# Kernel tuning notes

Measured on AMD Instinct MI355X. Metric: run time of the kernel, lower is better.

Reference implementation:

```python
import jax, jax.numpy as jnp
import numpy as np
import math

E = 256          # embed_dims
H = 8            # num_heads
ITER = 2         # iterative steps
PC_RANGE = (-140.8, -40.0, -3.0, 140.8, 40.0, 1.0)


def sine_embed(pos, num_feats):
    # pos: (..., 3) in (0,1); returns (..., 3*num_feats), per-coord interleaved sin/cos
    scale = 2.0 * math.pi
    i = jnp.arange(num_feats, dtype=jnp.float32)
    dim_t = 10000.0 ** (2.0 * jnp.floor(i / 2.0) / num_feats)
    p = pos[..., None] * scale / dim_t                      # (..., 3, F)
    emb = jnp.stack([jnp.sin(p[..., 0::2]), jnp.cos(p[..., 1::2])], axis=-1)
    emb = emb.reshape(p.shape[:-1] + (num_feats,))          # (..., 3, F)
    return emb.reshape(pos.shape[:-1] + (3 * num_feats,))


def mha(q, k, v, Wi, bi, Wo, bo, n_heads):
    # torch nn.MultiheadAttention math, seq-first layout: q (L,N,C), k/v (M,N,C)
    L, N, C = q.shape
    D = C // n_heads
    qp = (q @ Wi[:C].T + bi[:C]).reshape(L, N, n_heads, D)
    kp = (k @ Wi[C:2 * C].T + bi[C:2 * C]).reshape(k.shape[0], N, n_heads, D)
    vp = (v @ Wi[2 * C:].T + bi[2 * C:]).reshape(v.shape[0], N, n_heads, D)
    scores = jnp.einsum('lnhd,mnhd->nhlm', qp, kp) / math.sqrt(D)
    attn = jax.nn.softmax(scores, axis=-1)
    o = jnp.einsum('nhlm,mnhd->lnhd', attn, vp).reshape(L, N, C)
    return o @ Wo.T + bo


def setup_inputs() -> dict:
    key = jax.random.key(0)
    ks = jax.random.split(key, 12)
    Q, TOT, B, LMAX = 2048, 40, 8, 5
    s = 0.02
    return {
        'x': jax.random.normal(ks[0], (Q, TOT, E), jnp.float32),
        'reference_points': jax.random.uniform(ks[1], (TOT, Q, 3), jnp.float32),
        'pairwise_t_matrix': jax.random.normal(ks[2], (B, LMAX, LMAX, 4, 4), jnp.float32),
        'record_len': np.full((B,), 5, dtype=np.int64),
        'in_proj_w': jax.random.normal(ks[3], (3 * E, E), jnp.float32) * s,
        'in_proj_b': jnp.zeros((3 * E,), jnp.float32),
        'out_w': jax.random.normal(ks[4], (E, E), jnp.float32) * s,
        'out_b': jnp.zeros((E,), jnp.float32),
        'bev_w1': jax.random.normal(ks[5], (E, 3 * E), jnp.float32) * s,
        'bev_b1': jnp.zeros((E,), jnp.float32),
        'bev_w2': jax.random.normal(ks[6], (E, E), jnp.float32) * s,
        'bev_b2': jnp.zeros((E,), jnp.float32),
    }


def reference(x, reference_points, pairwise_t_matrix, in_proj_w, in_proj_b,
              out_w, out_b, bev_w1, bev_b1, bev_w2, bev_b2, record_len):
    rl = np.asarray(record_len)
    offsets = np.concatenate([[0], np.cumsum(rl)]).astype(int)
    lo = jnp.asarray(PC_RANGE[:3], jnp.float32)
    hi = jnp.asarray(PC_RANGE[3:], jnp.float32)

    x_cav = jnp.transpose(x, (1, 0, 2))                    # (total_cav, Q, C)
    ref = reference_points * (hi - lo) + lo                # un-normalize to pc_range

    outs = []
    for b in range(len(rl)):
        s, e = offsets[b], offsets[b + 1]
        n = e - s
        b_x = x_cav[s:e]                                   # (n, Q, C)
        if n == 1:
            outs.append(b_x)
            continue
        b_ref = ref[s:e]                                   # (n, Q, 3)
        t_ego = pairwise_t_matrix[b, :n, 0]                # (n, 4, 4) transform-to-ego
        homo = jnp.concatenate([b_ref, jnp.ones(b_ref.shape[:-1] + (1,), b_ref.dtype)], axis=-1)
        trans = jax.nn.sigmoid(jnp.einsum('nij,nqj->nqi', t_ego, homo)[..., :3])
        pe = sine_embed(trans, E)                          # (n, Q, 3E)
        bev = jax.nn.relu(pe @ bev_w1.T + bev_b1) @ bev_w2.T + bev_b2  # (n, Q, C)

        ego = b_x[0:1]
        neigh = b_x[1:]                                    # (n-1, Q, C)
        kk = neigh + bev[1:]
        for _ in range(ITER):
            q = jnp.broadcast_to(ego, neigh.shape)
            o = q + mha(q, kk, neigh, in_proj_w, in_proj_b, out_w, out_b, H)
            ego = jnp.sum(o, axis=0, keepdims=True)
        outs.append(jnp.concatenate([ego, neigh], axis=0))

    out = jnp.concatenate(outs, axis=0)                    # (total_cav, Q, C)
    return jnp.transpose(out, (1, 0, 2))                   # (Q, total_cav, C)
```

## Files before the change

### kernel.cpp

```cpp
#include <hip/hip_runtime.h>
#include <cstdint>
#include <cstddef>

typedef __bf16 bf16;
typedef __attribute__((ext_vector_type(8))) __bf16 bf16x8;
typedef __attribute__((ext_vector_type(4))) float f32x4;
typedef __attribute__((ext_vector_type(4))) unsigned int u32x4;

#define QN 2048

#if __has_builtin(__builtin_amdgcn_sinf)
#define SIN_REV(x) __builtin_amdgcn_sinf(x)
#define COS_REV(x) __builtin_amdgcn_cosf(x)
#else
#define SIN_REV(x) __sinf((x) * 6.283185307179586f)
#define COS_REV(x) __cosf((x) * 6.283185307179586f)
#endif

__device__ __forceinline__ float sigmoidf_(float v) { return 1.0f / (1.0f + __expf(-v)); }

__device__ __forceinline__ bf16x8 cvt8(const float* p) {
  const f32x4* p4 = (const f32x4*)p;
  f32x4 lo = p4[0], hi = p4[1];
  bf16x8 r;
#pragma unroll
  for (int j = 0; j < 4; ++j) { r[j] = (bf16)lo[j]; r[j + 4] = (bf16)hi[j]; }
  return r;
}

__device__ __forceinline__ void load_lds16(const bf16* g, bf16* l) {
  __builtin_amdgcn_global_load_lds(
      (const __attribute__((address_space(1))) void*)g,
      (__attribute__((address_space(3))) void*)l, 16, 0, 0);
}

__global__ __launch_bounds__(256) void copy_ker(const u32x4* __restrict__ in,
                                                u32x4* __restrict__ out, int n) {
  int i = blockIdx.x * 256 + threadIdx.x;
  if (i >= n) return;
  int t = (i >> 6) % 40;
  if ((t % 5) == 0) return;
  out[i] = in[i];
}

__global__ __launch_bounds__(256) void cvtw_ker(const float* __restrict__ ipw,
                                                const float* __restrict__ ow,
                                                const float* __restrict__ w1,
                                                const float* __restrict__ w2,
                                                bf16* __restrict__ wb) {
  int e = (blockIdx.x * 256 + threadIdx.x) * 8;
  const float* src; int off;
  if (e < 196608)      { src = ipw; off = e; }
  else if (e < 262144) { src = ow;  off = e - 196608; }
  else if (e < 458752) { src = w1;  off = e - 262144; }
  else                 { src = w2;  off = e - 458752; }
  *(bf16x8*)(wb + e) = cvt8(src + off);
}

__global__ __launch_bounds__(256) void wcomb_ker(const float* __restrict__ ipw,
                                                 const float* __restrict__ ipb,
                                                 const float* __restrict__ w2f,
                                                 const float* __restrict__ b2f,
                                                 bf16* __restrict__ Wc,
                                                 float* __restrict__ bkf) {
  __shared__ float row[256];
  __shared__ float red[256];
  const int j = blockIdx.x, l = threadIdx.x;
  row[l] = ipw[65536 + j * 256 + l];
  __syncthreads();
  float acc = 0.f;
#pragma unroll 4
  for (int m = 0; m < 256; ++m) acc += row[m] * w2f[m * 256 + l];
  Wc[(size_t)j * 512 + l] = (bf16)acc;
  Wc[(size_t)j * 512 + 256 + l] = (bf16)row[l];
  red[l] = row[l] * b2f[l];
  __syncthreads();
  for (int s = 128; s > 0; s >>= 1) {
    if (l < s) red[l] += red[l + s];
    __syncthreads();
  }
  if (l == 0) bkf[j] = ipb[256 + j] + red[0];
}

template <int AMODE, int EPI, int KDIM>
__global__ __launch_bounds__(256) void gemm_ker(
    const bf16* __restrict__ A, const float* __restrict__ Af,
    const bf16* __restrict__ W, const float* __restrict__ bias,
    const float* __restrict__ x, const float* __restrict__ rp,
    const float* __restrict__ pm, const float* __restrict__ egoPrev,
    bf16* __restrict__ outB, float* __restrict__ outF) {
  __shared__ bf16 As[128][40];
  __shared__ bf16 Bs[128][32];

  const int tid = threadIdx.x;
  const int bidm = blockIdx.x >> 1;
  const int bidn = blockIdx.x & 1;
  const int rowBase = bidm << 7;
  const int colBase = bidn << 7;

  const int wave = tid >> 6, lane = tid & 63;
  const int m16 = lane & 15, quad = lane >> 4;
  const int wr = wave >> 1, wc = wave & 1;

  const int sRow = tid >> 1, sHalf = tid & 1;
  const int rgA = rowBase + sRow;

  const float* afp = nullptr;
  float tr0 = 0.f, tr1 = 0.f, tr2 = 0.f;
  if constexpr (AMODE == 1) {
    int b = rgA >> 13, j = (rgA >> 11) & 3, q = rgA & 2047;
    int t = b * 5 + 1 + j;
    const float* rpp = rp + ((size_t)t * QN + q) * 3;
    float r0 = rpp[0] * 281.6f - 140.8f;
    float r1 = rpp[1] * 80.0f - 40.0f;
    float r2 = rpp[2] * 4.0f - 3.0f;
    const float* T = pm + (size_t)t * 80;
    tr0 = sigmoidf_(T[0] * r0 + T[1] * r1 + T[2] * r2 + T[3]);
    tr1 = sigmoidf_(T[4] * r0 + T[5] * r1 + T[6] * r2 + T[7]);
    tr2 = sigmoidf_(T[8] * r0 + T[9] * r1 + T[10] * r2 + T[11]);
  } else if constexpr (AMODE == 2 || AMODE == 5) {
    int b = rgA >> 13, j = (rgA >> 11) & 3, q = rgA & 2047;
    afp = x + (((size_t)q * 40 + b * 5 + 1 + j) << 8);
  } else if constexpr (AMODE == 3) {
    int b = rgA >> 11, q = rgA & 2047;
    afp = x + (((size_t)q * 40 + b * 5) << 8);
  } else if constexpr (AMODE == 4) {
    afp = Af + (size_t)rgA * 256;
  }

  const bf16* wsrc = W + (size_t)(colBase + (wave << 5) + (lane >> 2)) * KDIM + ((lane & 3) << 3);
  bf16* bdst0 = &Bs[(wave << 5)][0];
  bf16* bdst1 = &Bs[(wave << 5) + 16][0];

  f32x4 acc[4][4] = {};

  for (int k0 = 0; k0 < KDIM; k0 += 32) {
    load_lds16(wsrc + k0, bdst0);
    load_lds16(wsrc + (size_t)16 * KDIM + k0, bdst1);

    bf16x8 a0, a1;
    if constexpr (AMODE == 1) {
      int c = k0 >> 8;
      float tc = (c == 0) ? tr0 : (c == 1 ? tr1 : tr2);
      int ti0 = ((k0 & 255) + (sHalf << 4)) >> 1;
      float freq = exp2f((float)ti0 * -0.10381025296522975f);
#pragma unroll
      for (int p = 0; p < 4; ++p) {
        float ang = tc * freq;
        a0[2 * p]     = (bf16)SIN_REV(ang);
        a0[2 * p + 1] = (bf16)COS_REV(ang);
        freq *= 0.93057204092467f;
      }
#pragma unroll
      for (int p = 0; p < 4; ++p) {
        float ang = tc * freq;
        a1[2 * p]     = (bf16)SIN_REV(ang);
        a1[2 * p + 1] = (bf16)COS_REV(ang);
        freq *= 0.93057204092467f;
      }
    } else if constexpr (AMODE == 0) {
      const bf16* ap = A + (size_t)rgA * KDIM + k0 + (sHalf << 4);
      a0 = ((const bf16x8*)ap)[0];
      a1 = ((const bf16x8*)ap)[1];
    } else if constexpr (AMODE == 5) {
      if (k0 < 256) {
        const bf16* ap = A + ((size_t)rgA << 8) + k0 + (sHalf << 4);
        a0 = ((const bf16x8*)ap)[0];
        a1 = ((const bf16x8*)ap)[1];
      } else {
        const float* fp = afp + (k0 - 256) + (sHalf << 4);
        a0 = cvt8(fp);
        a1 = cvt8(fp + 8);
      }
    } else {
      const float* fp = afp + k0 + (sHalf << 4);
      a0 = cvt8(fp);
      a1 = cvt8(fp + 8);
    }
    *(bf16x8*)(&As[sRow][sHalf << 4]) = a0;
    *(bf16x8*)(&As[sRow][(sHalf << 4) + 8]) = a1;
    __syncthreads();

    bf16x8 afr[4], bfr[4];
#pragma unroll
    for (int mt = 0; mt < 4; ++mt)
      afr[mt] = *(const bf16x8*)(&As[(wr << 6) + (mt << 4) + m16][quad << 3]);
#pragma unroll
    for (int nt = 0; nt < 4; ++nt)
      bfr[nt] = *(const bf16x8*)(&Bs[(wc << 6) + (nt << 4) + m16][quad << 3]);
#pragma unroll
    for (int mt = 0; mt < 4; ++mt)
#pragma unroll
      for (int nt = 0; nt < 4; ++nt)
        acc[mt][nt] = __builtin_amdgcn_mfma_f32_16x16x32_bf16(
            afr[mt], bfr[nt], acc[mt][nt], 0, 0, 0);
    __syncthreads();
  }

#pragma unroll
  for (int mt = 0; mt < 4; ++mt) {
#pragma unroll
    for (int nt = 0; nt < 4; ++nt) {
      const int col = colBase + (wc << 6) + (nt << 4) + m16;
      const float bv = bias[col];
#pragma unroll
      for (int rg = 0; rg < 4; ++rg) {
        const int r = rowBase + (wr << 6) + (mt << 4) + (quad << 2) + rg;
        float v = acc[mt][nt][rg] + bv;
        if constexpr (EPI == 0) {
          outB[(size_t)r * 256 + col] = (bf16)fmaxf(v, 0.0f);
        } else if constexpr (EPI == 1) {
          int b = r >> 13, j = (r >> 11) & 3, q = r & 2047;
          v += x[(((size_t)q * 40 + b * 5 + 1 + j) << 8) + col];
          outB[(size_t)r * 256 + col] = (bf16)v;
        } else if constexpr (EPI == 2) {
          outB[(size_t)r * 256 + col] = (bf16)v;
        } else if constexpr (EPI == 3) {
          int b = r >> 11, q = r & 2047;
          float xe = x[(((size_t)q * 40 + b * 5) << 8) + col];
          outF[(size_t)r * 256 + col] = 4.0f * (xe + v);
        } else if constexpr (EPI == 4) {
          int b = r >> 11, q = r & 2047;
          float e1 = egoPrev[(size_t)r * 256 + col];
          outF[(((size_t)q * 40 + b * 5) << 8) + col] = 4.0f * (e1 + v);
        }
      }
    }
  }
}

__global__ __launch_bounds__(256) void attn_ker(const bf16* __restrict__ qp,
                                                const bf16* __restrict__ kp,
                                                const bf16* __restrict__ vp,
                                                bf16* __restrict__ o) {
  int p = blockIdx.x * 256 + threadIdx.x;
  int h = p & 7;
  int re = p >> 3;
  int b = re >> 11;
  int q = re & 2047;
  const bf16x8* qpv = (const bf16x8*)(qp + ((size_t)re << 8) + h * 32);
  float qv[32];
#pragma unroll
  for (int i = 0; i < 4; ++i) {
    bf16x8 t = qpv[i];
#pragma unroll
    for (int j = 0; j < 8; ++j) qv[i * 8 + j] = (float)t[j];
  }
  size_t base = ((size_t)(b * 4) * QN + q) * 256 + h * 32;
  float s[4];
#pragma unroll
  for (int m = 0; m < 4; ++m) {
    const bf16x8* kv = (const bf16x8*)(kp + base + (size_t)m * (QN * 256));
    float a = 0.f;
#pragma unroll
    for (int i = 0; i < 4; ++i) {
      bf16x8 t = kv[i];
#pragma unroll
      for (int j = 0; j < 8; ++j) a += qv[i * 8 + j] * (float)t[j];
    }
    s[m] = a * 0.17677669529663687f;
  }
  float mx = fmaxf(fmaxf(s[0], s[1]), fmaxf(s[2], s[3]));
  float e0 = __expf(s[0] - mx), e1 = __expf(s[1] - mx);
  float e2 = __expf(s[2] - mx), e3 = __expf(s[3] - mx);
  float inv = 1.0f / (e0 + e1 + e2 + e3);
  float w[4] = {e0 * inv, e1 * inv, e2 * inv, e3 * inv};
  float ov[32] = {};
#pragma unroll
  for (int m = 0; m < 4; ++m) {
    const bf16x8* vv = (const bf16x8*)(vp + base + (size_t)m * (QN * 256));
#pragma unroll
    for (int i = 0; i < 4; ++i) {
      bf16x8 t = vv[i];
#pragma unroll
      for (int j = 0; j < 8; ++j) ov[i * 8 + j] += w[m] * (float)t[j];
    }
  }
  bf16x8* op = (bf16x8*)(o + ((size_t)re << 8) + h * 32);
#pragma unroll
  for (int i = 0; i < 4; ++i) {
    bf16x8 t;
#pragma unroll
    for (int j = 0; j < 8; ++j) t[j] = (bf16)ov[i * 8 + j];
    op[i] = t;
  }
}

extern "C" void kernel_launch(void* const* d_in, const int* in_sizes, int n_in,
                              void* d_out, int out_size, void* d_ws, size_t ws_size,
                              hipStream_t stream) {
  (void)n_in; (void)out_size; (void)ws_size;
  const float* x   = (const float*)d_in[0];
  const float* rp  = (const float*)d_in[1];
  const float* pm  = (const float*)d_in[2];
  const int wbase = (in_sizes[3] == 8) ? 4 : 3;
  const float* ipw = (const float*)d_in[wbase + 0];
  const float* ipb = (const float*)d_in[wbase + 1];
  const float* ow  = (const float*)d_in[wbase + 2];
  const float* obv = (const float*)d_in[wbase + 3];
  const float* w1  = (const float*)d_in[wbase + 4];
  const float* b1  = (const float*)d_in[wbase + 5];
  const float* w2  = (const float*)d_in[wbase + 6];
  const float* b2  = (const float*)d_in[wbase + 7];
  float* out = (float*)d_out;
  char* ws = (char*)d_ws;

  bf16* h    = (bf16*)(ws + 0);
  bf16* qp   = (bf16*)(ws + 0);
  bf16* oo   = (bf16*)(ws + 8388608);
  bf16* kp   = (bf16*)(ws + 33554432);
  bf16* vp   = (bf16*)(ws + 67108864);
  float* egoF = (float*)(ws + 100663296);
  bf16* wb   = (bf16*)(ws + 117440512);
  bf16* Wc   = (bf16*)(ws + 118489088);
  float* bkf = (float*)(ws + 118751232);
  const bf16* wq  = wb;
  const bf16* wv  = wb + 131072;
  const bf16* owb = wb + 196608;
  const bf16* w1b = wb + 262144;

  cvtw_ker<<<256, 256, 0, stream>>>(ipw, ow, w1, w2, wb);
  wcomb_ker<<<256, 256, 0, stream>>>(ipw, ipb, w2, b2, Wc, bkf);
  copy_ker<<<20480, 256, 0, stream>>>((const u32x4*)x, (u32x4*)out, 5242880);
  gemm_ker<1, 0, 768><<<1024, 256, 0, stream>>>(nullptr, nullptr, w1b, b1, x, rp, pm, nullptr, h, nullptr);
  gemm_ker<5, 2, 512><<<1024, 256, 0, stream>>>(h, nullptr, Wc, bkf, x, rp, pm, nullptr, kp, nullptr);
  gemm_ker<2, 2, 256><<<1024, 256, 0, stream>>>(nullptr, nullptr, wv, ipb + 512, x, rp, pm, nullptr, vp, nullptr);
  gemm_ker<3, 2, 256><<<256, 256, 0, stream>>>(nullptr, nullptr, wq, ipb, x, rp, pm, nullptr, qp, nullptr);
  attn_ker<<<512, 256, 0, stream>>>(qp, kp, vp, oo);
  gemm_ker<0, 3, 256><<<256, 256, 0, stream>>>(oo, nullptr, owb, obv, x, rp, pm, nullptr, nullptr, egoF);
  gemm_ker<4, 2, 256><<<256, 256, 0, stream>>>(nullptr, egoF, wq, ipb, x, rp, pm, nullptr, qp, nullptr);
  attn_ker<<<512, 256, 0, stream>>>(qp, kp, vp, oo);
  gemm_ker<0, 4, 256><<<256, 256, 0, stream>>>(oo, nullptr, owb, obv, x, rp, pm, egoF, nullptr, out);
}
```

Baseline: 382.7 us.

## Build sine-embedding A fragments in registers for the PE GEMM, bypassing LDS

Replaces the generic GEMM's AMODE 1 path with a dedicated kernel for the positional-embedding MLP. Each lane generates its sin/cos values directly in MFMA A-fragment layout and reads weight fragments straight from global memory, so the kernel needs no LDS staging and no barriers. It also stops converting the unused w2 weight to bf16. The cost is duplicated transcendental work: both column-half waves compute the same rows. Weight reads now depend on cache behaviour rather than coalesced LDS staging.

```diff
diff --git a/kernel.cpp b/kernel.cpp
--- a/kernel.cpp
+++ b/kernel.cpp
@@ -46,14 +46,12 @@
 __global__ __launch_bounds__(256) void cvtw_ker(const float* __restrict__ ipw,
                                                 const float* __restrict__ ow,
                                                 const float* __restrict__ w1,
-                                                const float* __restrict__ w2,
                                                 bf16* __restrict__ wb) {
   int e = (blockIdx.x * 256 + threadIdx.x) * 8;
   const float* src; int off;
   if (e < 196608)      { src = ipw; off = e; }
   else if (e < 262144) { src = ow;  off = e - 196608; }
-  else if (e < 458752) { src = w1;  off = e - 262144; }
-  else                 { src = w2;  off = e - 458752; }
+  else                 { src = w1;  off = e - 262144; }
   *(bf16x8*)(wb + e) = cvt8(src + off);
 }
 
@@ -82,6 +80,91 @@
   if (l == 0) bkf[j] = ipb[256 + j] + red[0];
 }
 
+__global__ __launch_bounds__(256) void pe_gemm_ker(
+    const bf16* __restrict__ W, const float* __restrict__ bias,
+    const float* __restrict__ rp, const float* __restrict__ pm,
+    bf16* __restrict__ outB) {
+  const int tid = threadIdx.x;
+  const int bidm = blockIdx.x >> 1;
+  const int bidn = blockIdx.x & 1;
+  const int rowBase = bidm << 7;
+  const int colBase = bidn << 7;
+  const int wave = tid >> 6, lane = tid & 63;
+  const int m16 = lane & 15, quad = lane >> 4;
+  const int wr = wave >> 1, wc = wave & 1;
+
+  float tr[3][4];
+#pragma unroll
+  for (int mt = 0; mt < 4; ++mt) {
+    int r = rowBase + (wr << 6) + (mt << 4) + m16;
+    int b = r >> 13, j = (r >> 11) & 3, q = r & 2047;
+    int t = b * 5 + 1 + j;
+    const float* rpp = rp + ((size_t)t * QN + q) * 3;
+    float r0 = rpp[0] * 281.6f - 140.8f;
+    float r1 = rpp[1] * 80.0f - 40.0f;
+    float r2 = rpp[2] * 4.0f - 3.0f;
+    const float* T = pm + (size_t)t * 80;
+    tr[0][mt] = sigmoidf_(T[0] * r0 + T[1] * r1 + T[2] * r2 + T[3]);
+    tr[1][mt] = sigmoidf_(T[4] * r0 + T[5] * r1 + T[6] * r2 + T[7]);
+    tr[2][mt] = sigmoidf_(T[8] * r0 + T[9] * r1 + T[10] * r2 + T[11]);
+  }
+
+  const bf16* bsrc = W + (size_t)(colBase + (wc << 6) + m16) * 768 + (quad << 3);
+
+  const float freq0 = exp2f((float)(quad << 2) * -0.10381025296522975f);
+  const float R = 0.9305720409296979f;
+  const float R16 = 0.31622776601683794f;
+
+  f32x4 acc[4][4] = {};
+
+#pragma unroll
+  for (int c = 0; c < 3; ++c) {
+    float fq = freq0;
+#pragma unroll
+    for (int s = 0; s < 8; ++s) {
+      const int k0 = (c << 8) + (s << 5);
+      bf16x8 bfr[4];
+#pragma unroll
+      for (int nt = 0; nt < 4; ++nt)
+        bfr[nt] = *(const bf16x8*)(bsrc + (size_t)(nt << 4) * 768 + k0);
+      const float f0 = fq, f1 = f0 * R, f2 = f1 * R, f3 = f2 * R;
+      bf16x8 afr[4];
+#pragma unroll
+      for (int mt = 0; mt < 4; ++mt) {
+        const float tc = tr[c][mt];
+        const float a0 = tc * f0, a1 = tc * f1, a2 = tc * f2, a3 = tc * f3;
+        afr[mt][0] = (bf16)SIN_REV(a0); afr[mt][1] = (bf16)COS_REV(a0);
+        afr[mt][2] = (bf16)SIN_REV(a1); afr[mt][3] = (bf16)COS_REV(a1);
+        afr[mt][4] = (bf16)SIN_REV(a2); afr[mt][5] = (bf16)COS_REV(a2);
+        afr[mt][6] = (bf16)SIN_REV(a3); afr[mt][7] = (bf16)COS_REV(a3);
+      }
+#pragma unroll
+      for (int mt = 0; mt < 4; ++mt)
+#pragma unroll
+        for (int nt = 0; nt < 4; ++nt)
+          acc[mt][nt] = __builtin_amdgcn_mfma_f32_16x16x32_bf16(
+              afr[mt], bfr[nt], acc[mt][nt], 0, 0, 0);
+      fq = f3 * R * R16 / R16;
+      fq = f0 * R16;
+    }
+  }
+
+#pragma unroll
+  for (int mt = 0; mt < 4; ++mt) {
+#pragma unroll
+    for (int nt = 0; nt < 4; ++nt) {
+      const int col = colBase + (wc << 6) + (nt << 4) + m16;
+      const float bv = bias[col];
+#pragma unroll
+      for (int rg = 0; rg < 4; ++rg) {
+        const int r = rowBase + (wr << 6) + (mt << 4) + (quad << 2) + rg;
+        float v = acc[mt][nt][rg] + bv;
+        outB[(size_t)r * 256 + col] = (bf16)fmaxf(v, 0.0f);
+      }
+    }
+  }
+}
+
 template <int AMODE, int EPI, int KDIM>
 __global__ __launch_bounds__(256) void gemm_ker(
     const bf16* __restrict__ A, const float* __restrict__ Af,
@@ -106,19 +189,7 @@
   const int rgA = rowBase + sRow;
 
   const float* afp = nullptr;
-  float tr0 = 0.f, tr1 = 0.f, tr2 = 0.f;
-  if constexpr (AMODE == 1) {
-    int b = rgA >> 13, j = (rgA >> 11) & 3, q = rgA & 2047;
-    int t = b * 5 + 1 + j;
-    const float* rpp = rp + ((size_t)t * QN + q) * 3;
-    float r0 = rpp[0] * 281.6f - 140.8f;
-    float r1 = rpp[1] * 80.0f - 40.0f;
-    float r2 = rpp[2] * 4.0f - 3.0f;
-    const float* T = pm + (size_t)t * 80;
-    tr0 = sigmoidf_(T[0] * r0 + T[1] * r1 + T[2] * r2 + T[3]);
-    tr1 = sigmoidf_(T[4] * r0 + T[5] * r1 + T[6] * r2 + T[7]);
-    tr2 = sigmoidf_(T[8] * r0 + T[9] * r1 + T[10] * r2 + T[11]);
-  } else if constexpr (AMODE == 2 || AMODE == 5) {
+  if constexpr (AMODE == 2 || AMODE == 5) {
     int b = rgA >> 13, j = (rgA >> 11) & 3, q = rgA & 2047;
     afp = x + (((size_t)q * 40 + b * 5 + 1 + j) << 8);
   } else if constexpr (AMODE == 3) {
@@ -139,26 +210,7 @@
     load_lds16(wsrc + (size_t)16 * KDIM + k0, bdst1);
 
     bf16x8 a0, a1;
-    if constexpr (AMODE == 1) {
-      int c = k0 >> 8;
-      float tc = (c == 0) ? tr0 : (c == 1 ? tr1 : tr2);
-      int ti0 = ((k0 & 255) + (sHalf << 4)) >> 1;
-      float freq = exp2f((float)ti0 * -0.10381025296522975f);
-#pragma unroll
-      for (int p = 0; p < 4; ++p) {
-        float ang = tc * freq;
-        a0[2 * p]     = (bf16)SIN_REV(ang);
-        a0[2 * p + 1] = (bf16)COS_REV(ang);
-        freq *= 0.93057204092467f;
-      }
-#pragma unroll
-      for (int p = 0; p < 4; ++p) {
-        float ang = tc * freq;
-        a1[2 * p]     = (bf16)SIN_REV(ang);
-        a1[2 * p + 1] = (bf16)COS_REV(ang);
-        freq *= 0.93057204092467f;
-      }
-    } else if constexpr (AMODE == 0) {
+    if constexpr (AMODE == 0) {
       const bf16* ap = A + (size_t)rgA * KDIM + k0 + (sHalf << 4);
       a0 = ((const bf16x8*)ap)[0];
       a1 = ((const bf16x8*)ap)[1];
@@ -209,10 +261,6 @@
         float v = acc[mt][nt][rg] + bv;
         if constexpr (EPI == 0) {
           outB[(size_t)r * 256 + col] = (bf16)fmaxf(v, 0.0f);
-        } else if constexpr (EPI == 1) {
-          int b = r >> 13, j = (r >> 11) & 3, q = r & 2047;
-          v += x[(((size_t)q * 40 + b * 5 + 1 + j) << 8) + col];
-          outB[(size_t)r * 256 + col] = (bf16)v;
         } else if constexpr (EPI == 2) {
           outB[(size_t)r * 256 + col] = (bf16)v;
         } else if constexpr (EPI == 3) {
@@ -319,10 +367,10 @@
   const bf16* owb = wb + 196608;
   const bf16* w1b = wb + 262144;
 
-  cvtw_ker<<<256, 256, 0, stream>>>(ipw, ow, w1, w2, wb);
+  cvtw_ker<<<224, 256, 0, stream>>>(ipw, ow, w1, wb);
   wcomb_ker<<<256, 256, 0, stream>>>(ipw, ipb, w2, b2, Wc, bkf);
   copy_ker<<<20480, 256, 0, stream>>>((const u32x4*)x, (u32x4*)out, 5242880);
-  gemm_ker<1, 0, 768><<<1024, 256, 0, stream>>>(nullptr, nullptr, w1b, b1, x, rp, pm, nullptr, h, nullptr);
+  pe_gemm_ker<<<1024, 256, 0, stream>>>(w1b, b1, rp, pm, h);
   gemm_ker<5, 2, 512><<<1024, 256, 0, stream>>>(h, nullptr, Wc, bkf, x, rp, pm, nullptr, kp, nullptr);
   gemm_ker<2, 2, 256><<<1024, 256, 0, stream>>>(nullptr, nullptr, wv, ipb + 512, x, rp, pm, nullptr, vp, nullptr);
   gemm_ker<3, 2, 256><<<256, 256, 0, stream>>>(nullptr, nullptr, wq, ipb, x, rp, pm, nullptr, qp, nullptr);
```

Measured after the change: 414.7 us. 8.4% more time.

## Double-buffer GEMM with 256x64 tiles, XOR-swizzled LDS, and fuse x copy into V projection

Applied to the files above, without the earlier changes.

The GEMM kernel now uses 256x64 block tiles with a K-step of 64 and double-buffered, XOR-swizzled LDS. The next A/B slice is fetched into registers while MFMAs run on the current buffer, which halves barriers per K and is meant to hide global latency and avoid LDS bank conflicts. The separate copy kernel that wrote the neighbor rows of x into the output is removed. The V-projection GEMM now writes those fp32 rows while it reads them, and the unused w2 conversion is dropped. Costs are higher register pressure (launch_bounds 256,2) and larger LDS use, which may limit occupancy.

```diff
diff --git a/kernel.cpp b/kernel.cpp
--- a/kernel.cpp
+++ b/kernel.cpp
@@ -28,32 +28,28 @@
   return r;
 }
 
+__device__ __forceinline__ bf16x8 cvt8v(f32x4 lo, f32x4 hi) {
+  bf16x8 r;
+#pragma unroll
+  for (int j = 0; j < 4; ++j) { r[j] = (bf16)lo[j]; r[j + 4] = (bf16)hi[j]; }
+  return r;
+}
+
 __device__ __forceinline__ void load_lds16(const bf16* g, bf16* l) {
   __builtin_amdgcn_global_load_lds(
       (const __attribute__((address_space(1))) void*)g,
       (__attribute__((address_space(3))) void*)l, 16, 0, 0);
 }
 
-__global__ __launch_bounds__(256) void copy_ker(const u32x4* __restrict__ in,
-                                                u32x4* __restrict__ out, int n) {
-  int i = blockIdx.x * 256 + threadIdx.x;
-  if (i >= n) return;
-  int t = (i >> 6) % 40;
-  if ((t % 5) == 0) return;
-  out[i] = in[i];
-}
-
 __global__ __launch_bounds__(256) void cvtw_ker(const float* __restrict__ ipw,
                                                 const float* __restrict__ ow,
                                                 const float* __restrict__ w1,
-                                                const float* __restrict__ w2,
                                                 bf16* __restrict__ wb) {
   int e = (blockIdx.x * 256 + threadIdx.x) * 8;
   const float* src; int off;
   if (e < 196608)      { src = ipw; off = e; }
   else if (e < 262144) { src = ow;  off = e - 196608; }
-  else if (e < 458752) { src = w1;  off = e - 262144; }
-  else                 { src = w2;  off = e - 458752; }
+  else                 { src = w1;  off = e - 262144; }
   *(bf16x8*)(wb + e) = cvt8(src + off);
 }
 
@@ -82,28 +78,30 @@
   if (l == 0) bkf[j] = ipb[256 + j] + red[0];
 }
 
-template <int AMODE, int EPI, int KDIM>
-__global__ __launch_bounds__(256) void gemm_ker(
+template <int AMODE, int EPI, int KDIM, bool COPYX>
+__global__ __launch_bounds__(256, 2) void gemm_ker(
     const bf16* __restrict__ A, const float* __restrict__ Af,
     const bf16* __restrict__ W, const float* __restrict__ bias,
     const float* __restrict__ x, const float* __restrict__ rp,
     const float* __restrict__ pm, const float* __restrict__ egoPrev,
     bf16* __restrict__ outB, float* __restrict__ outF) {
-  __shared__ bf16 As[128][40];
-  __shared__ bf16 Bs[128][32];
+  __shared__ bf16 As[2][256][64];
+  __shared__ bf16 Bs[2][64][64];
+
+  constexpr int NS = KDIM / 64;
 
   const int tid = threadIdx.x;
-  const int bidm = blockIdx.x >> 1;
-  const int bidn = blockIdx.x & 1;
-  const int rowBase = bidm << 7;
-  const int colBase = bidn << 7;
+  const int bidm = blockIdx.x >> 2;
+  const int bidn = blockIdx.x & 3;
+  const int rowBase = bidm << 8;
+  const int colBase = bidn << 6;
 
   const int wave = tid >> 6, lane = tid & 63;
   const int m16 = lane & 15, quad = lane >> 4;
-  const int wr = wave >> 1, wc = wave & 1;
-
-  const int sRow = tid >> 1, sHalf = tid & 1;
-  const int rgA = rowBase + sRow;
+  const int sA = m16 & 7;
+  const int sT = tid & 7;
+
+  const int rgA = rowBase + tid;
 
   const float* afp = nullptr;
   float tr0 = 0.f, tr1 = 0.f, tr2 = 0.f;
@@ -127,92 +125,125 @@
   } else if constexpr (AMODE == 4) {
     afp = Af + (size_t)rgA * 256;
   }
-
-  const bf16* wsrc = W + (size_t)(colBase + (wave << 5) + (lane >> 2)) * KDIM + ((lane & 3) << 3);
-  bf16* bdst0 = &Bs[(wave << 5)][0];
-  bf16* bdst1 = &Bs[(wave << 5) + 16][0];
+  float* dstX = nullptr;
+  if constexpr (COPYX) dstX = outF + (afp - x);
+
+#define STAGE_B(PP, KO)                                                       \
+  {                                                                           \
+    _Pragma("unroll") for (int i_ = 0; i_ < 2; ++i_) {                        \
+      int rg_ = (wave << 3) + (i_ << 5) + (lane >> 3);                        \
+      const bf16* src_ = W + (size_t)(colBase + rg_) * KDIM + (KO) +          \
+                         (((lane & 7) ^ (lane >> 3)) << 3);                   \
+      load_lds16(src_, &Bs[(PP)][(wave << 3) + (i_ << 5)][0]);                \
+    }                                                                         \
+  }
+
+#define FETCH_A(KO)                                                           \
+  if constexpr (AMODE == 0) {                                                 \
+    _Pragma("unroll") for (int j_ = 0; j_ < 8; ++j_)                          \
+        aB[j_] = ((const bf16x8*)(A + (size_t)rgA * KDIM + (KO)))[j_];        \
+  } else if constexpr (AMODE == 5) {                                          \
+    if ((KO) < 256) {                                                         \
+      _Pragma("unroll") for (int j_ = 0; j_ < 8; ++j_)                        \
+          aB[j_] = ((const bf16x8*)(A + ((size_t)rgA << 8) + (KO)))[j_];      \
+    } else {                                                                  \
+      _Pragma("unroll") for (int j_ = 0; j_ < 16; ++j_)                       \
+          aF[j_] = ((const f32x4*)(afp + (KO) - 256))[j_];                    \
+    }                                                                         \
+  } else if constexpr (AMODE != 1) {                                          \
+    _Pragma("unroll") for (int j_ = 0; j_ < 16; ++j_)                         \
+        aF[j_] = ((const f32x4*)(afp + (KO)))[j_];                            \
+  }
+
+#define FINISH_A(PP, KO)                                                      \
+  {                                                                           \
+    bf16x8 v_[8];                                                             \
+    if constexpr (AMODE == 1) {                                               \
+      const int c_ = (KO) >> 8;                                               \
+      const float tc_ = (c_ == 0) ? tr0 : (c_ == 1 ? tr1 : tr2);              \
+      float fr_ = exp2f((float)(((KO) & 255) >> 1) * -0.10381025296522975f);  \
+      _Pragma("unroll") for (int js_ = 0; js_ < 32; ++js_) {                  \
+        float a_ = tc_ * fr_;                                                 \
+        v_[js_ >> 2][(js_ & 3) * 2] = (bf16)SIN_REV(a_);                      \
+        v_[js_ >> 2][(js_ & 3) * 2 + 1] = (bf16)COS_REV(a_);                  \
+        fr_ *= 0.9305720409296979f;                                           \
+      }                                                                       \
+    } else if constexpr (AMODE == 0) {                                        \
+      _Pragma("unroll") for (int j_ = 0; j_ < 8; ++j_) v_[j_] = aB[j_];       \
+    } else if constexpr (AMODE == 5) {                                        \
+      if ((KO) < 256) {                                                       \
+        _Pragma("unroll") for (int j_ = 0; j_ < 8; ++j_) v_[j_] = aB[j_];     \
+      } else {                                                                \
+        _Pragma("unroll") for (int j_ = 0; j_ < 8; ++j_)                      \
+            v_[j_] = cvt8v(aF[2 * j_], aF[2 * j_ + 1]);                       \
+      }                                                                       \
+    } else {                                                                  \
+      _Pragma("unroll") for (int j_ = 0; j_ < 8; ++j_)                        \
+          v_[j_] = cvt8v(aF[2 * j_], aF[2 * j_ + 1]);                         \
+      if constexpr (COPYX) {                                                  \
+        _Pragma("unroll") for (int j_ = 0; j_ < 16; ++j_)                     \
+            ((f32x4*)(dstX + (KO)))[j_] = aF[j_];                             \
+      }                                                                       \
+    }                                                                         \
+    _Pragma("unroll") for (int j_ = 0; j_ < 8; ++j_)                          \
+        *(bf16x8*)(&As[(PP)][tid][(j_ ^ sT) << 3]) = v_[j_];                  \
+  }
 
   f32x4 acc[4][4] = {};
 
-  for (int k0 = 0; k0 < KDIM; k0 += 32) {
-    load_lds16(wsrc + k0, bdst0);
-    load_lds16(wsrc + (size_t)16 * KDIM + k0, bdst1);
-
-    bf16x8 a0, a1;
-    if constexpr (AMODE == 1) {
-      int c = k0 >> 8;
-      float tc = (c == 0) ? tr0 : (c == 1 ? tr1 : tr2);
-      int ti0 = ((k0 & 255) + (sHalf << 4)) >> 1;
-      float freq = exp2f((float)ti0 * -0.10381025296522975f);
-#pragma unroll
-      for (int p = 0; p < 4; ++p) {
-        float ang = tc * freq;
-        a0[2 * p]     = (bf16)SIN_REV(ang);
-        a0[2 * p + 1] = (bf16)COS_REV(ang);
-        freq *= 0.93057204092467f;
-      }
-#pragma unroll
-      for (int p = 0; p < 4; ++p) {
-        float ang = tc * freq;
-        a1[2 * p]     = (bf16)SIN_REV(ang);
-        a1[2 * p + 1] = (bf16)COS_REV(ang);
-        freq *= 0.93057204092467f;
-      }
-    } else if constexpr (AMODE == 0) {
-      const bf16* ap = A + (size_t)rgA * KDIM + k0 + (sHalf << 4);
-      a0 = ((const bf16x8*)ap)[0];
-      a1 = ((const bf16x8*)ap)[1];
-    } else if constexpr (AMODE == 5) {
-      if (k0 < 256) {
-        const bf16* ap = A + ((size_t)rgA << 8) + k0 + (sHalf << 4);
-        a0 = ((const bf16x8*)ap)[0];
-        a1 = ((const bf16x8*)ap)[1];
-      } else {
-        const float* fp = afp + (k0 - 256) + (sHalf << 4);
-        a0 = cvt8(fp);
-        a1 = cvt8(fp + 8);
-      }
-    } else {
-      const float* fp = afp + k0 + (sHalf << 4);
-      a0 = cvt8(fp);
-      a1 = cvt8(fp + 8);
-    }
-    *(bf16x8*)(&As[sRow][sHalf << 4]) = a0;
-    *(bf16x8*)(&As[sRow][(sHalf << 4) + 8]) = a1;
+  {
+    f32x4 aF[16]; bf16x8 aB[8];
+    FETCH_A(0);
+    STAGE_B(0, 0);
+    FINISH_A(0, 0);
+  }
+  __syncthreads();
+
+#pragma unroll
+  for (int t = 0; t < NS; ++t) {
+    const int p = t & 1;
+    const int kn = (t + 1) << 6;
+    f32x4 aF[16]; bf16x8 aB[8];
+    if (t + 1 < NS) {
+      FETCH_A(kn);
+      STAGE_B(p ^ 1, kn);
+    }
+#pragma unroll
+    for (int kk = 0; kk < 2; ++kk) {
+      const int ks = (((kk << 2) + quad) ^ sA) << 3;
+      bf16x8 afr[4], bfr[4];
+#pragma unroll
+      for (int mt = 0; mt < 4; ++mt)
+        afr[mt] = *(const bf16x8*)(&As[p][(wave << 6) + (mt << 4) + m16][ks]);
+#pragma unroll
+      for (int nt = 0; nt < 4; ++nt)
+        bfr[nt] = *(const bf16x8*)(&Bs[p][(nt << 4) + m16][ks]);
+#pragma unroll
+      for (int mt = 0; mt < 4; ++mt)
+#pragma unroll
+        for (int nt = 0; nt < 4; ++nt)
+          acc[mt][nt] = __builtin_amdgcn_mfma_f32_16x16x32_bf16(
+              afr[mt], bfr[nt], acc[mt][nt], 0, 0, 0);
+    }
+    if (t + 1 < NS) FINISH_A(p ^ 1, kn);
     __syncthreads();
-
-    bf16x8 afr[4], bfr[4];
-#pragma unroll
-    for (int mt = 0; mt < 4; ++mt)
-      afr[mt] = *(const bf16x8*)(&As[(wr << 6) + (mt << 4) + m16][quad << 3]);
-#pragma unroll
-    for (int nt = 0; nt < 4; ++nt)
-      bfr[nt] = *(const bf16x8*)(&Bs[(wc << 6) + (nt << 4) + m16][quad << 3]);
-#pragma unroll
-    for (int mt = 0; mt < 4; ++mt)
-#pragma unroll
-      for (int nt = 0; nt < 4; ++nt)
-        acc[mt][nt] = __builtin_amdgcn_mfma_f32_16x16x32_bf16(
-            afr[mt], bfr[nt], acc[mt][nt], 0, 0, 0);
-    __syncthreads();
-  }
+  }
+#undef STAGE_B
+#undef FETCH_A
+#undef FINISH_A
 
 #pragma unroll
   for (int mt = 0; mt < 4; ++mt) {
 #pragma unroll
     for (int nt = 0; nt < 4; ++nt) {
-      const int col = colBase + (wc << 6) + (nt << 4) + m16;
+      const int col = colBase + (nt << 4) + m16;
       const float bv = bias[col];
 #pragma unroll
       for (int rg = 0; rg < 4; ++rg) {
-        const int r = rowBase + (wr << 6) + (mt << 4) + (quad << 2) + rg;
+        const int r = rowBase + (wave << 6) + (mt << 4) + (quad << 2) + rg;
         float v = acc[mt][nt][rg] + bv;
         if constexpr (EPI == 0) {
           outB[(size_t)r * 256 + col] = (bf16)fmaxf(v, 0.0f);
-        } else if constexpr (EPI == 1) {
-          int b = r >> 13, j = (r >> 11) & 3, q = r & 2047;
-          v += x[(((size_t)q * 40 + b * 5 + 1 + j) << 8) + col];
-          outB[(size_t)r * 256 + col] = (bf16)v;
         } else if constexpr (EPI == 2) {
           outB[(size_t)r * 256 + col] = (bf16)v;
         } else if constexpr (EPI == 3) {
@@ -319,16 +350,22 @@
   const bf16* owb = wb + 196608;
   const bf16* w1b = wb + 262144;
 
-  cvtw_ker<<<256, 256, 0, stream>>>(ipw, ow, w1, w2, wb);
+  cvtw_ker<<<224, 256, 0, stream>>>(ipw, ow, w1, wb);
   wcomb_ker<<<256, 256, 0, stream>>>(ipw, ipb, w2, b2, Wc, bkf);
-  copy_ker<<<20480, 256, 0, stream>>>((const u32x4*)x, (u32x4*)out, 5242880);
-  gemm_ker<1, 0, 768><<<1024, 256, 0, stream>>>(nullptr, nullptr, w1b, b1, x, rp, pm, nullptr, h, nullptr);
-  gemm_ker<5, 2, 512><<<1024, 256, 0, stream>>>(h, nullptr, Wc, bkf, x, rp, pm, nullptr, kp, nullptr);
-  gemm_ker<2, 2, 256><<<1024, 256, 0, stream>>>(nullptr, nullptr, wv, ipb + 512, x, rp, pm, nullptr, vp, nullptr);
-  gemm_ker<3, 2, 256><<<256, 256, 0, stream>>>(nullptr, nullptr, wq, ipb, x, rp, pm, nullptr, qp, nullptr);
+  gemm_ker<1, 0, 768, false><<<1024, 256, 0, stream>>>(
+      nullptr, nullptr, w1b, b1, x, rp, pm, nullptr, h, nullptr);
+  gemm_ker<5, 2, 512, false><<<1024, 256, 0, stream>>>(
+      h, nullptr, Wc, bkf, x, rp, pm, nullptr, kp, nullptr);
+  gemm_ker<2, 2, 256, true><<<1024, 256, 0, stream>>>(
+      nullptr, nullptr, wv, ipb + 512, x, rp, pm, nullptr, vp, out);
+  gemm_ker<3, 2, 256, false><<<256, 256, 0, stream>>>(
+      nullptr, nullptr, wq, ipb, x, rp, pm, nullptr, qp, nullptr);
   attn_ker<<<512, 256, 0, stream>>>(qp, kp, vp, oo);
-  gemm_ker<0, 3, 256><<<256, 256, 0, stream>>>(oo, nullptr, owb, obv, x, rp, pm, nullptr, nullptr, egoF);
-  gemm_ker<4, 2, 256><<<256, 256, 0, stream>>>(nullptr, egoF, wq, ipb, x, rp, pm, nullptr, qp, nullptr);
+  gemm_ker<0, 3, 256, false><<<256, 256, 0, stream>>>(
+      oo, nullptr, owb, obv, x, rp, pm, nullptr, nullptr, egoF);
+  gemm_ker<4, 2, 256, false><<<256, 256, 0, stream>>>(
+      nullptr, egoF, wq, ipb, x, rp, pm, nullptr, qp, nullptr);
   attn_ker<<<512, 256, 0, stream>>>(qp, kp, vp, oo);
-  gemm_ker<0, 4, 256><<<256, 256, 0, stream>>>(oo, nullptr, owb, obv, x, rp, pm, egoF, nullptr, out);
-}
+  gemm_ker<0, 4, 256, false><<<256, 256, 0, stream>>>(
+      oo, nullptr, owb, obv, x, rp, pm, egoF, nullptr, out);
+}
```

Result: slower. 519.8 us (+35.8%).

## Fuse both attention iterations into one kernel with LDS-resident ego rows

Applied to the files above, without the earlier changes.

Replaces the per-iteration sequence of Q-projection GEMM, attention kernel, output-projection GEMM (six launches) with a single kernel. Each block holds 32 ego rows in swizzled LDS and runs the q projection, attention, out projection and residual for both iterations. This removes the global round trips for qp, attention output and the ego intermediate, along with the launch overheads. In exchange, the small 32-row tiles reduce MFMA reuse of the weights, each block reloads the full weight matrices four times, and LDS usage is higher. The w2 conversion is dropped from the weight-conversion kernel because it was unused.

```diff
diff --git a/kernel.cpp b/kernel.cpp
--- a/kernel.cpp
+++ b/kernel.cpp
@@ -46,14 +46,12 @@
 __global__ __launch_bounds__(256) void cvtw_ker(const float* __restrict__ ipw,
                                                 const float* __restrict__ ow,
                                                 const float* __restrict__ w1,
-                                                const float* __restrict__ w2,
                                                 bf16* __restrict__ wb) {
   int e = (blockIdx.x * 256 + threadIdx.x) * 8;
   const float* src; int off;
   if (e < 196608)      { src = ipw; off = e; }
   else if (e < 262144) { src = ow;  off = e - 196608; }
-  else if (e < 458752) { src = w1;  off = e - 262144; }
-  else                 { src = w2;  off = e - 458752; }
+  else                 { src = w1;  off = e - 262144; }
   *(bf16x8*)(wb + e) = cvt8(src + off);
 }
 
@@ -84,11 +82,10 @@
 
 template <int AMODE, int EPI, int KDIM>
 __global__ __launch_bounds__(256) void gemm_ker(
-    const bf16* __restrict__ A, const float* __restrict__ Af,
-    const bf16* __restrict__ W, const float* __restrict__ bias,
-    const float* __restrict__ x, const float* __restrict__ rp,
-    const float* __restrict__ pm, const float* __restrict__ egoPrev,
-    bf16* __restrict__ outB, float* __restrict__ outF) {
+    const bf16* __restrict__ A, const bf16* __restrict__ W,
+    const float* __restrict__ bias, const float* __restrict__ x,
+    const float* __restrict__ rp, const float* __restrict__ pm,
+    bf16* __restrict__ outB) {
   __shared__ bf16 As[128][40];
   __shared__ bf16 Bs[128][32];
 
@@ -121,11 +118,6 @@
   } else if constexpr (AMODE == 2 || AMODE == 5) {
     int b = rgA >> 13, j = (rgA >> 11) & 3, q = rgA & 2047;
     afp = x + (((size_t)q * 40 + b * 5 + 1 + j) << 8);
-  } else if constexpr (AMODE == 3) {
-    int b = rgA >> 11, q = rgA & 2047;
-    afp = x + (((size_t)q * 40 + b * 5) << 8);
-  } else if constexpr (AMODE == 4) {
-    afp = Af + (size_t)rgA * 256;
   }
 
   const bf16* wsrc = W + (size_t)(colBase + (wave << 5) + (lane >> 2)) * KDIM + ((lane & 3) << 3);
@@ -209,44 +201,60 @@
         float v = acc[mt][nt][rg] + bv;
         if constexpr (EPI == 0) {
           outB[(size_t)r * 256 + col] = (bf16)fmaxf(v, 0.0f);
-        } else if constexpr (EPI == 1) {
-          int b = r >> 13, j = (r >> 11) & 3, q = r & 2047;
-          v += x[(((size_t)q * 40 + b * 5 + 1 + j) << 8) + col];
+        } else {
           outB[(size_t)r * 256 + col] = (bf16)v;
-        } else if constexpr (EPI == 2) {
-          outB[(size_t)r * 256 + col] = (bf16)v;
-        } else if constexpr (EPI == 3) {
-          int b = r >> 11, q = r & 2047;
-          float xe = x[(((size_t)q * 40 + b * 5) << 8) + col];
-          outF[(size_t)r * 256 + col] = 4.0f * (xe + v);
-        } else if constexpr (EPI == 4) {
-          int b = r >> 11, q = r & 2047;
-          float e1 = egoPrev[(size_t)r * 256 + col];
-          outF[(((size_t)q * 40 + b * 5) << 8) + col] = 4.0f * (e1 + v);
         }
       }
     }
   }
 }
 
-__global__ __launch_bounds__(256) void attn_ker(const bf16* __restrict__ qp,
-                                                const bf16* __restrict__ kp,
-                                                const bf16* __restrict__ vp,
-                                                bf16* __restrict__ o) {
-  int p = blockIdx.x * 256 + threadIdx.x;
-  int h = p & 7;
-  int re = p >> 3;
-  int b = re >> 11;
-  int q = re & 2047;
-  const bf16x8* qpv = (const bf16x8*)(qp + ((size_t)re << 8) + h * 32);
+__device__ __forceinline__ void proj32(const bf16 (*AP)[256], bf16 (*BsP)[32],
+                                       const bf16* __restrict__ WB,
+                                       f32x4 (*acc)[4], int wave, int lane) {
+  const int m16 = lane & 15, quad = lane >> 4;
+  for (int k0 = 0; k0 < 256; k0 += 32) {
+#pragma unroll
+    for (int i = 0; i < 4; ++i) {
+      const bf16* src = WB +
+          (size_t)((wave << 6) + (i << 4) + (lane >> 2)) * 256 + k0 +
+          ((lane & 3) << 3);
+      load_lds16(src, &BsP[(wave << 6) + (i << 4)][0]);
+    }
+    __syncthreads();
+    bf16x8 afr[2], bfr[4];
+#pragma unroll
+    for (int mt = 0; mt < 2; ++mt) {
+      const int r = (mt << 4) + m16;
+      afr[mt] = *(const bf16x8*)(&AP[r][(((k0 >> 3) + quad) ^ (r & 7)) << 3]);
+    }
+#pragma unroll
+    for (int nt = 0; nt < 4; ++nt)
+      bfr[nt] = *(const bf16x8*)(&BsP[(wave << 6) + (nt << 4) + m16][quad << 3]);
+#pragma unroll
+    for (int mt = 0; mt < 2; ++mt)
+#pragma unroll
+      for (int nt = 0; nt < 4; ++nt)
+        acc[mt][nt] = __builtin_amdgcn_mfma_f32_16x16x32_bf16(
+            afr[mt], bfr[nt], acc[mt][nt], 0, 0, 0);
+    __syncthreads();
+  }
+}
+
+__device__ __forceinline__ void attn_phase(bf16 (*P)[256],
+                                           const bf16* __restrict__ kp,
+                                           const bf16* __restrict__ vp,
+                                           int rowBase, int tid) {
+  const int r = tid >> 3, h = tid & 7;
+  const int re = rowBase + r, b = re >> 11, q = re & 2047;
   float qv[32];
 #pragma unroll
   for (int i = 0; i < 4; ++i) {
-    bf16x8 t = qpv[i];
+    bf16x8 t = *(const bf16x8*)(&P[r][((((h << 2) + i)) ^ (r & 7)) << 3]);
 #pragma unroll
     for (int j = 0; j < 8; ++j) qv[i * 8 + j] = (float)t[j];
   }
-  size_t base = ((size_t)(b * 4) * QN + q) * 256 + h * 32;
+  const size_t base = ((size_t)(b * 4) * QN + q) * 256 + h * 32;
   float s[4];
 #pragma unroll
   for (int m = 0; m < 4; ++m) {
@@ -276,14 +284,106 @@
       for (int j = 0; j < 8; ++j) ov[i * 8 + j] += w[m] * (float)t[j];
     }
   }
-  bf16x8* op = (bf16x8*)(o + ((size_t)re << 8) + h * 32);
 #pragma unroll
   for (int i = 0; i < 4; ++i) {
     bf16x8 t;
 #pragma unroll
     for (int j = 0; j < 8; ++j) t[j] = (bf16)ov[i * 8 + j];
-    op[i] = t;
-  }
+    *(bf16x8*)(&P[r][((((h << 2) + i)) ^ (r & 7)) << 3]) = t;
+  }
+}
+
+__global__ __launch_bounds__(256, 2) void iter_ker(
+    const bf16* __restrict__ kp, const bf16* __restrict__ vp,
+    const bf16* __restrict__ wq, const bf16* __restrict__ owb,
+    const float* __restrict__ qb, const float* __restrict__ ob,
+    const float* __restrict__ x, float* __restrict__ out) {
+  __shared__ bf16 P1[32][256];
+  __shared__ bf16 P2[32][256];
+  __shared__ bf16 Bs[256][32];
+
+  const int tid = threadIdx.x;
+  const int rowBase = blockIdx.x << 5;
+  const int wave = tid >> 6, lane = tid & 63;
+  const int m16 = lane & 15, quad = lane >> 4;
+
+  {
+    const int r = tid >> 3, e = tid & 7;
+    const int re = rowBase + r, b = re >> 11, q = re & 2047;
+    const float* src = x + (((size_t)q * 40 + b * 5) << 8) + (e << 5);
+#pragma unroll
+    for (int s = 0; s < 4; ++s) {
+      bf16x8 v = cvt8(src + s * 8);
+      *(bf16x8*)(&P1[r][((((e << 2) + s)) ^ (r & 7)) << 3]) = v;
+    }
+  }
+
+  float e1r[2][4][4];
+  f32x4 acc[2][4];
+
+#define ZACC                                                                  \
+  { _Pragma("unroll") for (int mt = 0; mt < 2; ++mt)                          \
+    _Pragma("unroll") for (int nt = 0; nt < 4; ++nt) {                        \
+      f32x4 z = {0.f, 0.f, 0.f, 0.f}; acc[mt][nt] = z; } }
+
+#define QEPI                                                                  \
+  { _Pragma("unroll") for (int mt = 0; mt < 2; ++mt)                          \
+    _Pragma("unroll") for (int nt = 0; nt < 4; ++nt) {                        \
+      const int col = (wave << 6) + (nt << 4) + m16;                          \
+      const float bv = qb[col];                                               \
+      _Pragma("unroll") for (int rg = 0; rg < 4; ++rg) {                      \
+        const int row = (mt << 4) + (quad << 2) + rg;                         \
+        P2[row][(((col >> 3) ^ (row & 7)) << 3) + (col & 7)] =                \
+            (bf16)(acc[mt][nt][rg] + bv);                                     \
+      } } }
+
+  ZACC;
+  proj32(P1, Bs, wq, acc, wave, lane);
+  QEPI;
+  __syncthreads();
+  attn_phase(P2, kp, vp, rowBase, tid);
+  ZACC;
+  proj32(P2, Bs, owb, acc, wave, lane);
+#pragma unroll
+  for (int mt = 0; mt < 2; ++mt)
+#pragma unroll
+    for (int nt = 0; nt < 4; ++nt) {
+      const int col = (wave << 6) + (nt << 4) + m16;
+      const float bv = ob[col];
+#pragma unroll
+      for (int rg = 0; rg < 4; ++rg) {
+        const int row = (mt << 4) + (quad << 2) + rg;
+        const int re = rowBase + row, b = re >> 11, q = re & 2047;
+        float xe = x[(((size_t)q * 40 + b * 5) << 8) + col];
+        float e1 = 4.0f * (xe + acc[mt][nt][rg] + bv);
+        e1r[mt][nt][rg] = e1;
+        P1[row][(((col >> 3) ^ (row & 7)) << 3) + (col & 7)] = (bf16)e1;
+      }
+    }
+
+  ZACC;
+  proj32(P1, Bs, wq, acc, wave, lane);
+  QEPI;
+  __syncthreads();
+  attn_phase(P2, kp, vp, rowBase, tid);
+  ZACC;
+  proj32(P2, Bs, owb, acc, wave, lane);
+#pragma unroll
+  for (int mt = 0; mt < 2; ++mt)
+#pragma unroll
+    for (int nt = 0; nt < 4; ++nt) {
+      const int col = (wave << 6) + (nt << 4) + m16;
+      const float bv = ob[col];
+#pragma unroll
+      for (int rg = 0; rg < 4; ++rg) {
+        const int row = (mt << 4) + (quad << 2) + rg;
+        const int re = rowBase + row, b = re >> 11, q = re & 2047;
+        out[(((size_t)q * 40 + b * 5) << 8) + col] =
+            4.0f * (e1r[mt][nt][rg] + acc[mt][nt][rg] + bv);
+      }
+    }
+#undef ZACC
+#undef QEPI
 }
 
 extern "C" void kernel_launch(void* const* d_in, const int* in_sizes, int n_in,
@@ -306,29 +406,21 @@
   char* ws = (char*)d_ws;
 
   bf16* h    = (bf16*)(ws + 0);
-  bf16* qp   = (bf16*)(ws + 0);
-  bf16* oo   = (bf16*)(ws + 8388608);
   bf16* kp   = (bf16*)(ws + 33554432);
   bf16* vp   = (bf16*)(ws + 67108864);
-  float* egoF = (float*)(ws + 100663296);
-  bf16* wb   = (bf16*)(ws + 117440512);
-  bf16* Wc   = (bf16*)(ws + 118489088);
-  float* bkf = (float*)(ws + 118751232);
+  bf16* wb   = (bf16*)(ws + 100663296);
+  bf16* Wc   = (bf16*)(ws + 101711872);
+  float* bkf = (float*)(ws + 101974016);
   const bf16* wq  = wb;
   const bf16* wv  = wb + 131072;
   const bf16* owb = wb + 196608;
   const bf16* w1b = wb + 262144;
 
-  cvtw_ker<<<256, 256, 0, stream>>>(ipw, ow, w1, w2, wb);
+  cvtw_ker<<<224, 256, 0, stream>>>(ipw, ow, w1, wb);
   wcomb_ker<<<256, 256, 0, stream>>>(ipw, ipb, w2, b2, Wc, bkf);
   copy_ker<<<20480, 256, 0, stream>>>((const u32x4*)x, (u32x4*)out, 5242880);
-  gemm_ker<1, 0, 768><<<1024, 256, 0, stream>>>(nullptr, nullptr, w1b, b1, x, rp, pm, nullptr, h, nullptr);
-  gemm_ker<5, 2, 512><<<1024, 256, 0, stream>>>(h, nullptr, Wc, bkf, x, rp, pm, nullptr, kp, nullptr);
-  gemm_ker<2, 2, 256><<<1024, 256, 0, stream>>>(nullptr, nullptr, wv, ipb + 512, x, rp, pm, nullptr, vp, nullptr);
-  gemm_ker<3, 2, 256><<<256, 256, 0, stream>>>(nullptr, nullptr, wq, ipb, x, rp, pm, nullptr, qp, nullptr);
-  attn_ker<<<512, 256, 0, stream>>>(qp, kp, vp, oo);
-  gemm_ker<0, 3, 256><<<256, 256, 0, stream>>>(oo, nullptr, owb, obv, x, rp, pm, nullptr, nullptr, egoF);
-  gemm_ker<4, 2, 256><<<256, 256, 0, stream>>>(nullptr, egoF, wq, ipb, x, rp, pm, nullptr, qp, nullptr);
-  attn_ker<<<512, 256, 0, stream>>>(qp, kp, vp, oo);
-  gemm_ker<0, 4, 256><<<256, 256, 0, stream>>>(oo, nullptr, owb, obv, x, rp, pm, egoF, nullptr, out);
-}
+  gemm_ker<1, 0, 768><<<1024, 256, 0, stream>>>(nullptr, w1b, b1, x, rp, pm, h);
+  gemm_ker<5, 2, 512><<<1024, 256, 0, stream>>>(h, Wc, bkf, x, rp, pm, kp);
+  gemm_ker<2, 2, 256><<<1024, 256, 0, stream>>>(nullptr, wv, ipb + 512, x, rp, pm, vp);
+  iter_ker<<<512, 256, 0, stream>>>(kp, vp, wq, owb, ipb, obv, x, out);
+}
```

Result: faster. 369.1 us (-3.6%).
